# Kernel optimization log

Hardware: AMD Instinct MI355X
Metric: run time of the kernel (lower is better)

## Reference

```python
import jax, jax.numpy as jnp
import numpy as np

N_HEAD = 16
LN_EPS = 1e-5


def _layernorm(x, g, b):
    mu = jnp.mean(x, axis=-1, keepdims=True)
    var = jnp.var(x, axis=-1, keepdims=True)
    return (x - mu) * jax.lax.rsqrt(var + LN_EPS) * g + b


def setup_inputs() -> dict:
    key = jax.random.key(0)
    ks = jax.random.split(key, 8)
    B, T, C = 8, 1024, 1024
    s = lambda fan_in: 1.0 / np.sqrt(fan_in)
    return {
        "x": jax.random.normal(ks[0], (B, T, C), jnp.float32),
        "kqv_w": jax.random.normal(ks[1], (3 * C, C), jnp.float32) * s(C),
        "kqv_b": jnp.zeros((3 * C,), jnp.float32),
        "proj_w": jax.random.normal(ks[2], (C, C), jnp.float32) * s(C),
        "proj_b": jnp.zeros((C,), jnp.float32),
        "ln1_g": jnp.ones((C,), jnp.float32),
        "ln1_b": jnp.zeros((C,), jnp.float32),
        "ln2_g": jnp.ones((C,), jnp.float32),
        "ln2_b": jnp.zeros((C,), jnp.float32),
        "fc1_w": jax.random.normal(ks[3], (4 * C, C), jnp.float32) * s(C),
        "fc1_b": jnp.zeros((4 * C,), jnp.float32),
        "fc2_w": jax.random.normal(ks[4], (C, 4 * C), jnp.float32) * s(4 * C),
        "fc2_b": jnp.zeros((C,), jnp.float32),
    }


def reference(x, kqv_w, kqv_b, proj_w, proj_b, ln1_g, ln1_b, ln2_g, ln2_b,
              fc1_w, fc1_b, fc2_w, fc2_b):
    B, T, C = x.shape
    hd = C // N_HEAD

    # --- attention sublayer ---
    h = _layernorm(x, ln1_g, ln1_b)
    kqv = h @ kqv_w.T + kqv_b                     # [B,T,3C]
    kqv = kqv.reshape(B, T, N_HEAD, 3 * hd)
    # ts.slice(kqv, 3, dim=-1) -> (k, q, v) in that order
    k = kqv[..., 0 * hd:1 * hd].transpose(0, 2, 1, 3)  # [B,H,T,hd]
    q = kqv[..., 1 * hd:2 * hd].transpose(0, 2, 1, 3)
    v = kqv[..., 2 * hd:3 * hd].transpose(0, 2, 1, 3)

    att = jnp.einsum('bhqd,bhkd->bhqk', q, k) * (1.0 / np.sqrt(hd))
    causal = jnp.tril(jnp.ones((T, T), dtype=bool))
    att = jnp.where(causal, att, jnp.float32(-jnp.inf))
    att = jax.nn.softmax(att, axis=-1)
    y = jnp.einsum('bhqk,bhkd->bhqd', att, v)     # [B,H,T,hd]
    y = y.transpose(0, 2, 1, 3).reshape(B, T, C)
    x = x + (y @ proj_w.T + proj_b)

    # --- MLP sublayer ---
    h = _layernorm(x, ln2_g, ln2_b)
    h = jax.nn.gelu(h @ fc1_w.T + fc1_b, approximate=False)  # nn.GELU exact
    x = x + (h @ fc2_w.T + fc2_b)
    return x
```

## Files before the change

kernel.cpp:

```cpp
#include <hip/hip_runtime.h>
#include <math.h>
#include <stdint.h>

typedef __bf16 bf16_t;
typedef __bf16 bf16x8 __attribute__((ext_vector_type(8)));
typedef float f32x4 __attribute__((ext_vector_type(4)));
typedef unsigned short ushort8_t __attribute__((ext_vector_type(8)));
typedef unsigned short ushort4_t __attribute__((ext_vector_type(4)));

#define LOG2E 1.44269504088896340736f

__device__ inline unsigned short f2bf_bits(float f) {
  union { float f; unsigned int u; } v; v.f = f;
  unsigned int u = v.u;
  return (unsigned short)((u + 0x7fffu + ((u >> 16) & 1u)) >> 16);
}

__device__ inline void gld_lds16(const void* g, void* l) {
  __builtin_amdgcn_global_load_lds(
      (__attribute__((address_space(1))) void*)(uintptr_t)(g),
      (__attribute__((address_space(3))) void*)(uintptr_t)(l),
      16, 0, 0);
}

#define BAR() __builtin_amdgcn_s_barrier()
#define LGKM0() asm volatile("s_waitcnt lgkmcnt(0)" ::: "memory")
#define VMW(n) asm volatile("s_waitcnt vmcnt(" #n ")" ::: "memory")
#define PRIO(p) __builtin_amdgcn_s_setprio(p)

__global__ __launch_bounds__(256) void cast_kernel(const float* __restrict__ in,
                                                   unsigned short* __restrict__ out,
                                                   int n) {
  int i = (blockIdx.x * 256 + threadIdx.x) * 4;
  if (i >= n) return;
  float4 f = *reinterpret_cast<const float4*>(in + i);
  ushort4_t o;
  o[0] = f2bf_bits(f.x); o[1] = f2bf_bits(f.y);
  o[2] = f2bf_bits(f.z); o[3] = f2bf_bits(f.w);
  *reinterpret_cast<ushort4_t*>(out + i) = o;
}

__global__ __launch_bounds__(256) void ln_kernel(const float* __restrict__ x,
                                                 const float* __restrict__ g,
                                                 const float* __restrict__ bta,
                                                 unsigned short* __restrict__ out) {
  const int row = blockIdx.x;
  const int c = threadIdx.x * 4;
  const float4 xv = *reinterpret_cast<const float4*>(x + (size_t)row * 1024 + c);
  float s = xv.x + xv.y + xv.z + xv.w;
  float sq = xv.x * xv.x + xv.y * xv.y + xv.z * xv.z + xv.w * xv.w;
#pragma unroll
  for (int xm = 1; xm < 64; xm <<= 1) {
    s += __shfl_xor(s, xm, 64);
    sq += __shfl_xor(sq, xm, 64);
  }
  __shared__ float sh[8];
  const int wave = threadIdx.x >> 6, lane = threadIdx.x & 63;
  if (lane == 0) { sh[wave] = s; sh[4 + wave] = sq; }
  __syncthreads();
  const float ts = sh[0] + sh[1] + sh[2] + sh[3];
  const float tq = sh[4] + sh[5] + sh[6] + sh[7];
  const float mean = ts * (1.0f / 1024.0f);
  const float var = tq * (1.0f / 1024.0f) - mean * mean;
  const float rstd = rsqrtf(var + 1e-5f);
  const float4 gv = *reinterpret_cast<const float4*>(g + c);
  const float4 bv = *reinterpret_cast<const float4*>(bta + c);
  ushort4_t o;
  o[0] = f2bf_bits((xv.x - mean) * rstd * gv.x + bv.x);
  o[1] = f2bf_bits((xv.y - mean) * rstd * gv.y + bv.y);
  o[2] = f2bf_bits((xv.z - mean) * rstd * gv.z + bv.z);
  o[3] = f2bf_bits((xv.w - mean) * rstd * gv.w + bv.w);
  *reinterpret_cast<ushort4_t*>(out + (size_t)row * 1024 + c) = o;
}

#define LDAF(SL)                                                              \
  do {                                                                        \
    _Pragma("unroll") for (int mi_ = 0; mi_ < 4; ++mi_)                       \
    _Pragma("unroll") for (int kh_ = 0; kh_ < 2; ++kh_) {                     \
      const int row_ = wm * 64 + mi_ * 16 + lr16;                             \
      af[mi_][kh_] = *reinterpret_cast<const bf16x8*>(                        \
          &lds[(SL) * ASLOT + row_ * 64 + ((kh_ * 32 + lk * 8) ^ axor)]);     \
    }                                                                         \
  } while (0)

#define LDBF(SL, HALF)                                                        \
  do {                                                                        \
    _Pragma("unroll") for (int n2_ = 0; n2_ < 2; ++n2_)                       \
    _Pragma("unroll") for (int kh_ = 0; kh_ < 2; ++kh_) {                     \
      const int row_ = wn * 64 + ((HALF) * 2 + n2_) * 16 + lr16;              \
      bf[n2_][kh_] = *reinterpret_cast<const bf16x8*>(                        \
          &lds[B0 + (SL) * BSLOT + row_ * 64 + ((kh_ * 32 + lk * 8) ^ axor)]); \
    }                                                                         \
  } while (0)

#define PMMA(HALF)                                                            \
  do {                                                                        \
    _Pragma("unroll") for (int mi_ = 0; mi_ < 4; ++mi_)                       \
    _Pragma("unroll") for (int n2_ = 0; n2_ < 2; ++n2_)                       \
    _Pragma("unroll") for (int kh_ = 0; kh_ < 2; ++kh_)                       \
      acc[mi_][(HALF) * 2 + n2_] = __builtin_amdgcn_mfma_f32_16x16x32_bf16(   \
          af[mi_][kh_], bf[n2_][kh_], acc[mi_][(HALF) * 2 + n2_], 0, 0, 0);   \
  } while (0)

template <int EPI>
__global__ __launch_bounds__(512) void gemm8(const unsigned short* __restrict__ A,
                                             const unsigned short* __restrict__ W,
                                             const float* __restrict__ bias,
                                             const float* __restrict__ res,
                                             unsigned short* __restrict__ outb,
                                             float* __restrict__ outf,
                                             int N, int K) {
  __shared__ unsigned short lds[3 * (128 + 256) * 64];
  const int tid = threadIdx.x;
  const int w = tid >> 6, l = tid & 63;
  const int m0 = blockIdx.y * 128, n0 = blockIdx.x * 256;
  const int wm = w >> 2, wn = w & 3;
  const int lr16 = l & 15, lk = l >> 4;
  const int axor = (lr16 & 7) << 3;

  const int ASLOT = 128 * 64;
  const int B0 = 3 * ASLOT;
  const int BSLOT = 256 * 64;

  const int sr = tid >> 3;
  const int sx = ((tid & 7) ^ (sr & 7)) << 3;
  auto stA = [&](int t, int s, int h) {
    gld_lds16(A + (size_t)(m0 + h * 64 + sr) * K + t * 64 + sx,
              &lds[s * ASLOT + h * 4096 + tid * 8]);
  };
  auto stB = [&](int t, int s, int c) {
    gld_lds16(W + (size_t)(n0 + c * 64 + sr) * K + t * 64 + sx,
              &lds[B0 + s * BSLOT + c * 4096 + tid * 8]);
  };

  f32x4 acc[4][4];
#pragma unroll
  for (int i = 0; i < 4; ++i)
#pragma unroll
    for (int j = 0; j < 4; ++j) { f32x4 z = {0.f, 0.f, 0.f, 0.f}; acc[i][j] = z; }
  bf16x8 af[4][2], bf[2][2];

  stA(0, 0, 0); stA(0, 0, 1);
  stB(0, 0, 0); stB(0, 0, 1); stB(0, 0, 2); stB(0, 0, 3);
  stA(1, 1, 0); stA(1, 1, 1);
  stB(1, 1, 0); stB(1, 1, 1); stB(1, 1, 2); stB(1, 1, 3);
  VMW(6);
  BAR();

  const int nt = K / 64;
  int s = 0;
  int sp = 2;
  for (int t = 0; t < nt - 2; ++t) {
    const int tp2 = t + 2;
    LDAF(s); LDBF(s, 0);
    stA(tp2, sp, 0); stA(tp2, sp, 1);
    stB(tp2, sp, 0); stB(tp2, sp, 1);
    BAR(); LGKM0(); PRIO(1); PMMA(0); PRIO(0); BAR();
    LDBF(s, 1);
    stB(tp2, sp, 2); stB(tp2, sp, 3);
    BAR(); LGKM0(); PRIO(1); PMMA(1); PRIO(0);
    VMW(6);
    BAR();
    s = (s == 2) ? 0 : s + 1;
    sp = (sp == 2) ? 0 : sp + 1;
  }
  LDAF(s); LDBF(s, 0);
  BAR(); LGKM0(); PRIO(1); PMMA(0); PRIO(0); BAR();
  LDBF(s, 1);
  BAR(); LGKM0(); PRIO(1); PMMA(1); PRIO(0);
  VMW(0);
  BAR();
  s = (s == 2) ? 0 : s + 1;
  LDAF(s); LDBF(s, 0);
  BAR(); LGKM0(); PRIO(1); PMMA(0); PRIO(0); BAR();
  LDBF(s, 1);
  LGKM0(); PRIO(1); PMMA(1); PRIO(0);

#pragma unroll
  for (int ni = 0; ni < 4; ++ni) {
    const int col = n0 + wn * 64 + ni * 16 + lr16;
    const float bv = bias[col];
#pragma unroll
    for (int mi = 0; mi < 4; ++mi) {
#pragma unroll
      for (int r = 0; r < 4; ++r) {
        const int row = m0 + wm * 64 + mi * 16 + lk * 4 + r;
        const size_t idx = (size_t)row * N + col;
        float v = acc[mi][ni][r] + bv;
        if (EPI == 0) {
          outb[idx] = f2bf_bits(v);
        } else if (EPI == 1) {
          outf[idx] = v + res[idx];
        } else {
          v = 0.5f * v * (1.0f + erff(v * 0.70710678118654752f));
          outb[idx] = f2bf_bits(v);
        }
      }
    }
  }
}

__device__ inline int swz(int row, int colelem) {
  return row * 64 + (colelem ^ ((row & 7) << 3));
}

__global__ __launch_bounds__(256) void attn_kernel(const unsigned short* __restrict__ kqv,
                                                   unsigned short* __restrict__ y) {
  __shared__ unsigned short Ks[2][64 * 64];
  __shared__ unsigned short Vt[2][64 * 64];
  __shared__ unsigned short Ps[4][16 * 64];

  const int tid = threadIdx.x;
  const int wave = tid >> 6;
  const int lane = tid & 63;
  const int bh = blockIdx.x;
  const int pair = blockIdx.y;
  const int b = bh >> 4;
  const int h = bh & 15;
  const int lo = pair;
  const int hi = 15 - pair;
  const int bT = b * 1024;
  const int hoff = h * 192;

  auto loadq = [&](int q0t, bf16x8 (&qf)[2]) {
    const unsigned short* qp =
        kqv + (size_t)(bT + q0t + wave * 16 + (lane & 15)) * 3072 + hoff + 64 +
        (lane >> 4) * 8;
#pragma unroll
    for (int kk = 0; kk < 2; ++kk) {
      bf16x8 t = *reinterpret_cast<const bf16x8*>(qp + kk * 32);
#pragma unroll
      for (int e = 0; e < 8; ++e) t[e] = (bf16_t)((float)t[e] * 0.125f);
      qf[kk] = t;
    }
  };

  auto stageK = [&](int j0, int bufi) {
#pragma unroll
    for (int i = 0; i < 2; ++i) {
      const int off = i * 4096 + wave * 1024 + lane * 16;
      const int jr = off >> 7;
      const int ce = ((off & 127) >> 1) ^ ((jr & 7) << 3);
      gld_lds16(kqv + (size_t)(bT + j0 + jr) * 3072 + hoff + ce,
                &Ks[bufi][i * 2048 + wave * 512]);
    }
  };

  ushort8_t vreg0, vreg1;
  auto vload = [&](int j0) {
    const unsigned short* vp =
        kqv + (size_t)(bT + j0 + (tid & 63)) * 3072 + hoff + 128 + (tid >> 6) * 8;
    vreg0 = *reinterpret_cast<const ushort8_t*>(vp);
    vreg1 = *reinterpret_cast<const ushort8_t*>(vp + 32);
  };
  auto vwrite = [&](int bufi) {
    const int j = tid & 63;
    const int dg = tid >> 6;
#pragma unroll
    for (int e = 0; e < 8; ++e) Vt[bufi][swz(dg * 8 + e, j)] = vreg0[e];
#pragma unroll
    for (int e = 0; e < 8; ++e) Vt[bufi][swz((dg + 4) * 8 + e, j)] = vreg1[e];
  };

  auto compute = [&](const bf16x8 (&qf)[2], f32x4 (&acc_o)[4], float (&mr)[4],
                     float (&lr)[4], int q0t, int j0, bool diag, int cur) {
    f32x4 s[4];
#pragma unroll
    for (int nt = 0; nt < 4; ++nt) {
      f32x4 a = {0.f, 0.f, 0.f, 0.f};
#pragma unroll
      for (int kk = 0; kk < 2; ++kk) {
        const bf16x8 kf = *reinterpret_cast<const bf16x8*>(
            &Ks[cur][swz(nt * 16 + (lane & 15), kk * 32 + (lane >> 4) * 8)]);
        a = __builtin_amdgcn_mfma_f32_16x16x32_bf16(qf[kk], kf, a, 0, 0, 0);
      }
      s[nt] = a;
    }
#pragma unroll
    for (int r = 0; r < 4; ++r) {
      float mx = -1e30f;
      if (diag) {
        const int qg = q0t + wave * 16 + ((lane >> 4) << 2) + r;
#pragma unroll
        for (int nt = 0; nt < 4; ++nt) {
          const int jg = j0 + nt * 16 + (lane & 15);
          const float sv = (jg <= qg) ? s[nt][r] : -1e30f;
          s[nt][r] = sv;
          mx = fmaxf(mx, sv);
        }
      } else {
#pragma unroll
        for (int nt = 0; nt < 4; ++nt) mx = fmaxf(mx, s[nt][r]);
      }
#pragma unroll
      for (int xm = 1; xm < 16; xm <<= 1) mx = fmaxf(mx, __shfl_xor(mx, xm, 64));
      const float mnew = fmaxf(mr[r], mx);
      const float sc = exp2f((mr[r] - mnew) * LOG2E);
      mr[r] = mnew;
      float ssum = 0.f;
#pragma unroll
      for (int nt = 0; nt < 4; ++nt) {
        const float p = exp2f((s[nt][r] - mnew) * LOG2E);
        s[nt][r] = p;
        ssum += p;
      }
#pragma unroll
      for (int xm = 1; xm < 16; xm <<= 1) ssum += __shfl_xor(ssum, xm, 64);
      lr[r] = lr[r] * sc + ssum;
#pragma unroll
      for (int dt = 0; dt < 4; ++dt) acc_o[dt][r] *= sc;
    }
    unsigned short* Pw = &Ps[wave][0];
#pragma unroll
    for (int nt = 0; nt < 4; ++nt)
#pragma unroll
      for (int r = 0; r < 4; ++r)
        Pw[swz(((lane >> 4) << 2) + r, nt * 16 + (lane & 15))] = f2bf_bits(s[nt][r]);
#pragma unroll
    for (int kk = 0; kk < 2; ++kk) {
      const bf16x8 pf = *reinterpret_cast<const bf16x8*>(
          &Ps[wave][swz(lane & 15, kk * 32 + (lane >> 4) * 8)]);
#pragma unroll
      for (int dt = 0; dt < 4; ++dt) {
        const bf16x8 vf = *reinterpret_cast<const bf16x8*>(
            &Vt[cur][swz(dt * 16 + (lane & 15), kk * 32 + (lane >> 4) * 8)]);
        acc_o[dt] = __builtin_amdgcn_mfma_f32_16x16x32_bf16(pf, vf, acc_o[dt], 0, 0, 0);
      }
    }
  };

  auto writeo = [&](int q0t, f32x4 (&acc_o)[4], float (&lr)[4]) {
#pragma unroll
    for (int dt = 0; dt < 4; ++dt)
#pragma unroll
      for (int r = 0; r < 4; ++r) {
        const int qg = q0t + wave * 16 + ((lane >> 4) << 2) + r;
        y[(size_t)(bT + qg) * 1024 + h * 64 + dt * 16 + (lane & 15)] =
            f2bf_bits(acc_o[dt][r] / lr[r]);
      }
  };

  bf16x8 qf_l[2], qf_h[2];
  loadq(lo * 64, qf_l);
  loadq(hi * 64, qf_h);
  f32x4 acc_l[4], acc_h[4];
#pragma unroll
  for (int dt = 0; dt < 4; ++dt) {
    f32x4 z = {0.f, 0.f, 0.f, 0.f};
    acc_l[dt] = z;
    acc_h[dt] = z;
  }
  float mr_l[4] = {-1e30f, -1e30f, -1e30f, -1e30f};
  float mr_h[4] = {-1e30f, -1e30f, -1e30f, -1e30f};
  float lr_l[4] = {0.f, 0.f, 0.f, 0.f};
  float lr_h[4] = {0.f, 0.f, 0.f, 0.f};

  stageK(0, 0);
  vload(0);
  vwrite(0);

  for (int jt = 0; jt <= hi; ++jt) {
    const int cur = jt & 1;
    __syncthreads();
    if (jt < hi) {
      stageK((jt + 1) * 64, cur ^ 1);
      vload((jt + 1) * 64);
    }
    compute(qf_h, acc_h, mr_h, lr_h, hi * 64, jt * 64, jt == hi, cur);
    if (jt <= lo)
      compute(qf_l, acc_l, mr_l, lr_l, lo * 64, jt * 64, jt == lo, cur);
    if (jt < hi) vwrite(cur ^ 1);
  }

  writeo(hi * 64, acc_h, lr_h);
  writeo(lo * 64, acc_l, lr_l);
}

extern "C" void kernel_launch(void* const* d_in, const int* in_sizes, int n_in,
                              void* d_out, int out_size, void* d_ws, size_t ws_size,
                              hipStream_t stream) {
  const float* x = (const float*)d_in[0];
  const float* kqv_w = (const float*)d_in[1];
  const float* kqv_b = (const float*)d_in[2];
  const float* proj_w = (const float*)d_in[3];
  const float* proj_b = (const float*)d_in[4];
  const float* ln1_g = (const float*)d_in[5];
  const float* ln1_b = (const float*)d_in[6];
  const float* ln2_g = (const float*)d_in[7];
  const float* ln2_b = (const float*)d_in[8];
  const float* fc1_w = (const float*)d_in[9];
  const float* fc1_b = (const float*)d_in[10];
  const float* fc2_w = (const float*)d_in[11];
  const float* fc2_b = (const float*)d_in[12];
  float* out = (float*)d_out;

  char* ws = (char*)d_ws;
  size_t off = 0;
  auto alloc = [&](size_t bytes) {
    char* p = ws + off;
    off += (bytes + 255) & ~(size_t)255;
    return p;
  };
  unsigned short* wk = (unsigned short*)alloc((size_t)3072 * 1024 * 2);
  unsigned short* wp = (unsigned short*)alloc((size_t)1024 * 1024 * 2);
  unsigned short* w1 = (unsigned short*)alloc((size_t)4096 * 1024 * 2);
  unsigned short* w2 = (unsigned short*)alloc((size_t)4096 * 1024 * 2);
  unsigned short* hbuf = (unsigned short*)alloc((size_t)8192 * 1024 * 2);
  unsigned short* kqvb = (unsigned short*)alloc((size_t)8192 * 3072 * 2);
  unsigned short* yb = (unsigned short*)alloc((size_t)8192 * 1024 * 2);
  float* x1 = (float*)alloc((size_t)8192 * 1024 * 4);
  unsigned short* a1 = (unsigned short*)alloc((size_t)8192 * 4096 * 2);

  cast_kernel<<<dim3(3072 * 1024 / 1024), 256, 0, stream>>>(kqv_w, wk, 3072 * 1024);
  cast_kernel<<<dim3(1024 * 1024 / 1024), 256, 0, stream>>>(proj_w, wp, 1024 * 1024);
  cast_kernel<<<dim3(4096 * 1024 / 1024), 256, 0, stream>>>(fc1_w, w1, 4096 * 1024);
  cast_kernel<<<dim3(4096 * 1024 / 1024), 256, 0, stream>>>(fc2_w, w2, 4096 * 1024);

  ln_kernel<<<dim3(8192), 256, 0, stream>>>(x, ln1_g, ln1_b, hbuf);

  gemm8<0><<<dim3(3072 / 256, 8192 / 128), 512, 0, stream>>>(
      hbuf, wk, kqv_b, nullptr, kqvb, nullptr, 3072, 1024);

  attn_kernel<<<dim3(128, 8), 256, 0, stream>>>(kqvb, yb);

  gemm8<1><<<dim3(1024 / 256, 8192 / 128), 512, 0, stream>>>(
      yb, wp, proj_b, x, nullptr, x1, 1024, 1024);

  ln_kernel<<<dim3(8192), 256, 0, stream>>>(x1, ln2_g, ln2_b, hbuf);

  gemm8<2><<<dim3(4096 / 256, 8192 / 128), 512, 0, stream>>>(
      hbuf, w1, fc1_b, nullptr, a1, nullptr, 4096, 1024);

  gemm8<1><<<dim3(1024 / 256, 8192 / 128), 512, 0, stream>>>(
      a1, w2, fc2_b, x1, nullptr, out, 1024, 4096);
}
```

Measured before the change: 445.6 us.

## Add 256x256-tile 16-wave GEMM with double buffering for QKV and FC1

Introduces a gemm16 kernel that uses 1024-thread blocks computing 256x256 output tiles, with a two-stage LDS double buffer instead of the three-stage pipeline in gemm8. It is used for the QKV and FC1 projections, where N is large, to double A-tile reuse per block and halve the number of blocks. The trade-off is 128 KB of LDS per block and a full vmcnt(0) wait each iteration, which exposes more global-load latency and limits occupancy to one block per CU.

```diff
diff --git a/kernel.cpp b/kernel.cpp
--- a/kernel.cpp
+++ b/kernel.cpp
@@ -148,8 +148,7 @@
   BAR();
 
   const int nt = K / 64;
-  int s = 0;
-  int sp = 2;
+  int s = 0, sp = 2;
   for (int t = 0; t < nt - 2; ++t) {
     const int tp2 = t + 2;
     LDAF(s); LDBF(s, 0);
@@ -175,6 +174,87 @@
   BAR(); LGKM0(); PRIO(1); PMMA(0); PRIO(0); BAR();
   LDBF(s, 1);
   LGKM0(); PRIO(1); PMMA(1); PRIO(0);
+
+#pragma unroll
+  for (int ni = 0; ni < 4; ++ni) {
+    const int col = n0 + wn * 64 + ni * 16 + lr16;
+    const float bv = bias[col];
+#pragma unroll
+    for (int mi = 0; mi < 4; ++mi) {
+#pragma unroll
+      for (int r = 0; r < 4; ++r) {
+        const int row = m0 + wm * 64 + mi * 16 + lk * 4 + r;
+        const size_t idx = (size_t)row * N + col;
+        float v = acc[mi][ni][r] + bv;
+        if (EPI == 0) {
+          outb[idx] = f2bf_bits(v);
+        } else if (EPI == 1) {
+          outf[idx] = v + res[idx];
+        } else {
+          v = 0.5f * v * (1.0f + erff(v * 0.70710678118654752f));
+          outb[idx] = f2bf_bits(v);
+        }
+      }
+    }
+  }
+}
+
+template <int EPI>
+__global__ __launch_bounds__(1024) void gemm16(const unsigned short* __restrict__ A,
+                                               const unsigned short* __restrict__ W,
+                                               const float* __restrict__ bias,
+                                               const float* __restrict__ res,
+                                               unsigned short* __restrict__ outb,
+                                               float* __restrict__ outf,
+                                               int N, int K) {
+  __shared__ unsigned short lds[2 * (256 + 256) * 64];
+  const int tid = threadIdx.x;
+  const int w = tid >> 6, l = tid & 63;
+  const int m0 = blockIdx.y * 256, n0 = blockIdx.x * 256;
+  const int wm = w >> 2, wn = w & 3;
+  const int lr16 = l & 15, lk = l >> 4;
+  const int axor = (lr16 & 7) << 3;
+
+  const int ASLOT = 256 * 64;
+  const int B0 = 2 * ASLOT;
+  const int BSLOT = 256 * 64;
+
+  const int sr = tid >> 3;
+  const int sx = ((tid & 7) ^ (sr & 7)) << 3;
+  auto stA = [&](int t, int s, int h) {
+    gld_lds16(A + (size_t)(m0 + h * 128 + sr) * K + t * 64 + sx,
+              &lds[s * ASLOT + h * 8192 + tid * 8]);
+  };
+  auto stB = [&](int t, int s, int h) {
+    gld_lds16(W + (size_t)(n0 + h * 128 + sr) * K + t * 64 + sx,
+              &lds[B0 + s * BSLOT + h * 8192 + tid * 8]);
+  };
+
+  f32x4 acc[4][4];
+#pragma unroll
+  for (int i = 0; i < 4; ++i)
+#pragma unroll
+    for (int j = 0; j < 4; ++j) { f32x4 z = {0.f, 0.f, 0.f, 0.f}; acc[i][j] = z; }
+  bf16x8 af[4][2], bf[2][2];
+
+  stA(0, 0, 0); stA(0, 0, 1);
+  stB(0, 0, 0); stB(0, 0, 1);
+  VMW(0);
+  BAR();
+
+  const int nt = K / 64;
+  for (int t = 0; t < nt; ++t) {
+    const int cur = t & 1;
+    const bool pf = (t + 1 < nt);
+    LDAF(cur); LDBF(cur, 0);
+    if (pf) { stA(t + 1, cur ^ 1, 0); stA(t + 1, cur ^ 1, 1); }
+    BAR(); LGKM0(); PRIO(1); PMMA(0); PRIO(0); BAR();
+    LDBF(cur, 1);
+    if (pf) { stB(t + 1, cur ^ 1, 0); stB(t + 1, cur ^ 1, 1); }
+    BAR(); LGKM0(); PRIO(1); PMMA(1); PRIO(0);
+    VMW(0);
+    BAR();
+  }
 
 #pragma unroll
   for (int ni = 0; ni < 4; ++ni) {
@@ -418,7 +498,7 @@
 
   ln_kernel<<<dim3(8192), 256, 0, stream>>>(x, ln1_g, ln1_b, hbuf);
 
-  gemm8<0><<<dim3(3072 / 256, 8192 / 128), 512, 0, stream>>>(
+  gemm16<0><<<dim3(3072 / 256, 8192 / 256), 1024, 0, stream>>>(
       hbuf, wk, kqv_b, nullptr, kqvb, nullptr, 3072, 1024);
 
   attn_kernel<<<dim3(128, 8), 256, 0, stream>>>(kqvb, yb);
@@ -428,7 +508,7 @@
 
   ln_kernel<<<dim3(8192), 256, 0, stream>>>(x1, ln2_g, ln2_b, hbuf);
 
-  gemm8<2><<<dim3(4096 / 256, 8192 / 128), 512, 0, stream>>>(
+  gemm16<2><<<dim3(4096 / 256, 8192 / 256), 1024, 0, stream>>>(
       hbuf, w1, fc1_b, nullptr, a1, nullptr, 4096, 1024);
 
   gemm8<1><<<dim3(1024 / 256, 8192 / 128), 512, 0, stream>>>(
```

New measurement: 466.0 us. 1.05x slower.
